# Kernel tuning notes

Hardware: AMD Instinct MI355X
Metric: run time of the kernel (lower is better)

The kernel has to match this reference:

```python
import jax, jax.numpy as jnp
import numpy as np

N_PAIR = 45  # n_agents=10 -> 10*9/2
TINY_THR = np.sqrt(np.finfo(np.float32).tiny).astype(np.float32) * N_PAIR


def setup_inputs() -> dict:
    key = jax.random.key(0)
    ks = jax.random.split(key, 8)
    bs, T, din, H = 4096, 64, 512, 64
    s = lambda fan: 1.0 / np.sqrt(fan)
    return {
        "main": jax.random.normal(ks[0], (1, bs, T, din), jnp.float32),
        "hidden_states": jnp.zeros((1, bs, 1, H), jnp.float32),
        "epsilons": jax.random.uniform(ks[1], (bs, 1), jnp.float32),
        "W_fc1": jax.random.normal(ks[2], (H, din), jnp.float32) * s(din),
        "b_fc1": jnp.zeros((H,), jnp.float32),
        "W_ih": jax.random.normal(ks[3], (3 * H, H), jnp.float32) * s(H),
        "W_hh": jax.random.normal(ks[4], (3 * H, H), jnp.float32) * s(H),
        "b_ih": jnp.zeros((3 * H,), jnp.float32),
        "b_hh": jnp.zeros((3 * H,), jnp.float32),
        "W_out": jax.random.normal(ks[5], (N_PAIR, H), jnp.float32) * s(H),
        "b_out": jnp.zeros((N_PAIR,), jnp.float32),
    }


def reference(main, hidden_states, epsilons, W_fc1, b_fc1, W_ih, W_hh, b_ih, b_hh, W_out, b_out):
    x = main[0]                       # [bs, T, din]
    h0 = hidden_states[0, :, 0, :]    # [bs, H]
    H = h0.shape[-1]

    # Encoder: fc1 + relu (time-independent, fully batched)
    enc = jax.nn.relu(jnp.einsum('bti,oi->bto', x, W_fc1) + b_fc1)  # [bs,T,H]
    # Precompute input-side GRU gates for all timesteps
    gi = jnp.einsum('bth,gh->btg', enc, W_ih) + b_ih                # [bs,T,3H]
    gi_t = jnp.transpose(gi, (1, 0, 2))                             # [T,bs,3H]

    def step(h, g_in):
        gh = h @ W_hh.T + b_hh
        i_r, i_z, i_n = jnp.split(g_in, 3, axis=-1)
        h_r, h_z, h_n = jnp.split(gh, 3, axis=-1)
        r = jax.nn.sigmoid(i_r + h_r)
        z = jax.nn.sigmoid(i_z + h_z)
        n = jnp.tanh(i_n + r * h_n)
        h_new = (1.0 - z) * n + z * h
        return h_new, h_new

    _, hs = jax.lax.scan(step, h0, gi_t)          # hs: [T,bs,H]
    hs = jnp.transpose(hs, (1, 0, 2))             # [bs,T,H]

    # Output head + custom exp-normalize with zero-sum guard
    logits = jnp.einsum('bth,oh->bto', hs, W_out) + b_out  # [bs,T,N_PAIR]
    p = jnp.exp(logits)
    p_sum = jnp.sum(p, axis=-1, keepdims=True)
    p_sum = jnp.where(p_sum <= TINY_THR, 1.0, p_sum)
    p = p / p_sum

    # Epsilon-greedy mixing (softmax exploration, not test_mode)
    eps = epsilons[:, None, :]                    # [bs,1,1]
    p = eps / N_PAIR + p * (1.0 - eps)

    x_out = p[None]                               # [1,bs,T,N_PAIR]
    h_out = hs[None]                              # [1,bs,T,H]
    return (x_out, h_out)
```

## Files before the change

### kernel.cpp

```cpp
#include <hip/hip_runtime.h>

typedef __attribute__((ext_vector_type(4))) float  f32x4;
typedef __attribute__((ext_vector_type(4))) __bf16 bf16x4;
typedef __attribute__((ext_vector_type(8))) __bf16 bf16x8;

#define MFMA16 __builtin_amdgcn_mfma_f32_16x16x32_bf16
#define TINY_THR 4.8789098e-18f
#define XOUT_N ((size_t)4096 * 64 * 45)

__device__ __forceinline__ void bar_lds() {
  asm volatile("s_waitcnt lgkmcnt(0)\n\ts_barrier" ::: "memory");
}
__device__ __forceinline__ void split_bf16(float v, __bf16& h, __bf16& l) {
  h = (__bf16)v; l = (__bf16)(v - (float)h);
}
__device__ __forceinline__ void gll16(const void* g, void* l) {
  __builtin_amdgcn_global_load_lds(
      (const __attribute__((address_space(1))) void*)g,
      (__attribute__((address_space(3))) void*)l, 16, 0, 0);
}

__device__ __forceinline__ int pk_off(int row, int col) {
  const int kk = col >> 5, rem = col & 31;
  const int half = rem >> 4, qq = (rem >> 2) & 3, j = rem & 3;
  return row * 128 + ((((kk << 2) | qq) ^ (row & 7)) << 4) + half * 8 + j * 2;
}
__device__ __forceinline__ bf16x8 frag_pk(const char* base, int row, int kk, int qq) {
  return *(const bf16x8*)(base + row * 128 + ((((kk << 2) | qq) ^ (row & 7)) << 4));
}

__global__ void k_prepW(const float* __restrict__ Wfc, __bf16* __restrict__ Wpk) {
  const int idx = blockIdx.x * 256 + threadIdx.x;
  const float v = Wfc[idx];
  __bf16 h, l; split_bf16(v, h, l);
  const int row = idx >> 9, k = idx & 511;
  const int c = k >> 6, kl = k & 63;
  const int kk = kl >> 5, rem = kl & 31;
  const int half = rem >> 4, q = (rem >> 2) & 3, j = rem & 3;
  const int blk = ((kk << 2) | q) ^ (row & 7);
  const int pos = c * 8192 + row * 64 + blk * 8 + half * 4 + j;
  Wpk[pos] = h;
  Wpk[pos + 4096] = l;
}

__global__ __launch_bounds__(256, 2) void k_encgemm(
    const float* __restrict__ x, const __bf16* __restrict__ Wpk,
    const float* __restrict__ bfc, float* __restrict__ enc) {
  __shared__ __attribute__((aligned(16))) char sm[65536];
  const int tid  = threadIdx.x;
  const int lane = tid & 63;
  const int wv   = tid >> 6;
  const int fr   = lane & 15;
  const int q    = lane >> 4;
  const int b    = blockIdx.x;

  auto stage = [&](int c, int buf) {
    char* xbase = sm + buf * 16384;
    char* wbase = sm + 32768 + buf * 16384;
    #pragma unroll
    for (int i = 0; i < 4; ++i) {
      const int B   = wv * 256 + i * 64 + lane;
      const int row = B >> 4, blk = B & 15;
      const int bp  = blk ^ (row & 15);
      const int colb = ((bp >> 3) << 5) | ((bp & 1) << 4) | (((bp >> 1) & 3) << 2);
      const float* src = x + ((size_t)b * 64 + row) * 512 + c * 64 + colb;
      gll16(src, xbase + wv * 4096 + i * 1024);
    }
    #pragma unroll
    for (int i = 0; i < 4; ++i) {
      const __bf16* srcw = Wpk + c * 8192 + wv * 2048 + i * 512 + lane * 8;
      gll16(srcw, wbase + wv * 4096 + i * 1024);
    }
  };

  f32x4 acc[4];
  #pragma unroll
  for (int nt = 0; nt < 4; ++nt) acc[nt] = (f32x4){0.f, 0.f, 0.f, 0.f};

  stage(0, 0);
  int buf = 0;
  for (int c = 0; c < 8; ++c) {
    if (c < 7) {
      stage(c + 1, buf ^ 1);
      asm volatile("s_waitcnt vmcnt(8)\n\ts_barrier" ::: "memory");
    } else {
      asm volatile("s_waitcnt vmcnt(0)\n\ts_barrier" ::: "memory");
    }
    const char* xbase = sm + buf * 16384;
    const char* wbase = sm + 32768 + buf * 16384;
    const int arow = wv * 16 + fr;
    bf16x8 Ah[2], Al[2];
    #pragma unroll
    for (int kk = 0; kk < 2; ++kk) {
      f32x4 u0 = *(const f32x4*)(xbase + arow * 256 + (((kk * 8 + q * 2 + 0) ^ (arow & 15)) << 4));
      f32x4 u1 = *(const f32x4*)(xbase + arow * 256 + (((kk * 8 + q * 2 + 1) ^ (arow & 15)) << 4));
      #pragma unroll
      for (int j = 0; j < 4; ++j) {
        __bf16 h, l;
        split_bf16(u0[j], h, l); Ah[kk][j] = h;     Al[kk][j] = l;
        split_bf16(u1[j], h, l); Ah[kk][4 + j] = h; Al[kk][4 + j] = l;
      }
    }
    #pragma unroll
    for (int nt = 0; nt < 4; ++nt) {
      const int brow = nt * 16 + fr;
      #pragma unroll
      for (int kk = 0; kk < 2; ++kk) {
        bf16x8 Bh = frag_pk(wbase, brow, kk, q);
        bf16x8 Bl = frag_pk(wbase + 8192, brow, kk, q);
        acc[nt] = MFMA16(Ah[kk], Bh, acc[nt], 0, 0, 0);
        acc[nt] = MFMA16(Ah[kk], Bl, acc[nt], 0, 0, 0);
        acc[nt] = MFMA16(Al[kk], Bh, acc[nt], 0, 0, 0);
      }
    }
    bar_lds();
    buf ^= 1;
  }
  #pragma unroll
  for (int nt = 0; nt < 4; ++nt) {
    const int o = nt * 16 + fr;
    const float bb = bfc[o];
    #pragma unroll
    for (int e = 0; e < 4; ++e) {
      const int t = wv * 16 + q * 4 + e;
      float v = acc[nt][e] + bb;
      enc[((size_t)b * 64 + t) * 64 + o] = fmaxf(v, 0.f);
    }
  }
}

__global__ __launch_bounds__(512, 1) void k_scan(
    const float* __restrict__ enc, const float* __restrict__ h0g,
    const float* __restrict__ eps, const float* __restrict__ Wih,
    const float* __restrict__ Whh, const float* __restrict__ bih,
    const float* __restrict__ bhh, const float* __restrict__ Wout,
    const float* __restrict__ bout, float* __restrict__ xout,
    float* __restrict__ hout) {
  __shared__ __attribute__((aligned(16))) char sm[55808];
  char* const wst0 = sm;
  char* const wst1 = sm + 24576;

  const int tid  = threadIdx.x;
  const int lane = tid & 63;
  const int wv   = tid >> 6;
  const int fr   = lane & 15;
  const int q    = lane >> 4;
  const int bbase = blockIdx.x * 16;
  const bool isB = (wv < 4);
  const int aw  = wv - 4;
  const int at  = tid & 255;
  const int sb  = at >> 4;
  const int sub = at & 15;
  const int so  = sub << 2;

  float hreg[4] = {0.f, 0.f, 0.f, 0.f};
  float biasNh = 0.f;
  int hcol = 0;
  float bR_ = 0.f, bZ_ = 0.f, bN_ = 0.f, boutv = 0.f, epsv = 0.f;
  if (isB) {
    hcol = wv * 16 + fr;
    biasNh = bhh[128 + hcol];
    #pragma unroll
    for (int e = 0; e < 4; ++e)
      hreg[e] = h0g[(size_t)(bbase + q * 4 + e) * 64 + hcol];
  } else {
    const int gc = aw * 16 + fr;
    bR_ = bih[gc] + bhh[gc];
    bZ_ = bih[64 + gc] + bhh[64 + gc];
    bN_ = bih[128 + gc];
    if (aw < 3 && gc < 45) boutv = bout[gc];
    epsv = eps[bbase + sb];
  }

  bf16x8 Fh[3][2], Fl[3][2];
  bf16x8 Fout[2][2];

  for (int idx = tid; idx < 192 * 64; idx += 512) {
    __bf16 h, l; split_bf16(Wih[idx], h, l);
    const int off = pk_off(idx >> 6, idx & 63);
    *(__bf16*)(wst0 + off) = h;
    *(__bf16*)(wst1 + off) = l;
  }
  bar_lds();
  if (!isB) {
    #pragma unroll
    for (int t3 = 0; t3 < 3; ++t3)
      #pragma unroll
      for (int kk = 0; kk < 2; ++kk) {
        const int row = (aw + 4 * t3) * 16 + fr;
        Fh[t3][kk] = frag_pk(wst0, row, kk, q);
        Fl[t3][kk] = frag_pk(wst1, row, kk, q);
      }
  }
  bar_lds();
  for (int idx = tid; idx < 192 * 64; idx += 512) {
    __bf16 h, l; split_bf16(Whh[idx], h, l);
    const int off = pk_off(idx >> 6, idx & 63);
    *(__bf16*)(wst0 + off) = h;
    *(__bf16*)(wst1 + off) = l;
  }
  bar_lds();
  if (isB) {
    #pragma unroll
    for (int t3 = 0; t3 < 3; ++t3)
      #pragma unroll
      for (int kk = 0; kk < 2; ++kk) {
        const int row = (wv + 4 * t3) * 16 + fr;
        Fh[t3][kk] = frag_pk(wst0, row, kk, q);
        Fl[t3][kk] = frag_pk(wst1, row, kk, q);
      }
  }
  bar_lds();
  for (int idx = tid; idx < 48 * 64; idx += 512) {
    float v = (idx < 45 * 64) ? Wout[idx] : 0.f;
    __bf16 h, l; split_bf16(v, h, l);
    const int off = pk_off(idx >> 6, idx & 63);
    *(__bf16*)(wst0 + off) = h;
    *(__bf16*)(wst1 + off) = l;
  }
  bar_lds();
  if (!isB && aw < 3) {
    #pragma unroll
    for (int kk = 0; kk < 2; ++kk) {
      const int row = aw * 16 + fr;
      Fout[kk][0] = frag_pk(wst0, row, kk, q);
      Fout[kk][1] = frag_pk(wst1, row, kk, q);
    }
  }
  bar_lds();

  auto gate_mfma = [&](const char* s0, f32x4& a0, f32x4& a1, f32x4& a2) {
    const char* s1 = s0 + 2048;
    bf16x8 Sh[2], Sl[2];
    #pragma unroll
    for (int kk = 0; kk < 2; ++kk) {
      Sh[kk] = frag_pk(s0, fr, kk, q);
      Sl[kk] = frag_pk(s1, fr, kk, q);
    }
    __builtin_amdgcn_s_setprio(1);
    #pragma unroll
    for (int kk = 0; kk < 2; ++kk) {
      a0 = MFMA16(Sh[kk], Fh[0][kk], a0, 0, 0, 0);
      a0 = MFMA16(Sh[kk], Fl[0][kk], a0, 0, 0, 0);
      a0 = MFMA16(Sl[kk], Fh[0][kk], a0, 0, 0, 0);
      a1 = MFMA16(Sh[kk], Fh[1][kk], a1, 0, 0, 0);
      a1 = MFMA16(Sh[kk], Fl[1][kk], a1, 0, 0, 0);
      a1 = MFMA16(Sl[kk], Fh[1][kk], a1, 0, 0, 0);
      a2 = MFMA16(Sh[kk], Fh[2][kk], a2, 0, 0, 0);
      a2 = MFMA16(Sh[kk], Fl[2][kk], a2, 0, 0, 0);
      a2 = MFMA16(Sl[kk], Fh[2][kk], a2, 0, 0, 0);
    }
    __builtin_amdgcn_s_setprio(0);
  };
  auto put_epd = [&](int dst, const f32x4& ev) {
    bf16x4 h4, l4;
    #pragma unroll
    for (int j = 0; j < 4; ++j) { __bf16 h, l; split_bf16(ev[j], h, l); h4[j] = h; l4[j] = l; }
    char* p0 = sm + 8192 + dst * 4096;
    const int off = pk_off(sb, so);
    *(bf16x4*)(p0 + off) = h4;
    *(bf16x4*)(p0 + 2048 + off) = l4;
  };
  auto put_gi = [&](int dst, const f32x4& a0, const f32x4& a1, const f32x4& a2) {
    float* gw = (float*)(sm + 16384 + dst * 16640);
    const int gc = aw * 16 + fr;
    #pragma unroll
    for (int e = 0; e < 4; ++e) {
      f32x4 o = (f32x4){a0[e] + bR_, a1[e] + bZ_, a2[e] + bN_, 0.f};
      *(f32x4*)(gw + (q * 4 + e) * 260 + gc * 4) = o;
    }
  };

  f32x4 evA = (f32x4){0.f,0.f,0.f,0.f}, evB = evA, e1v = evA;
  if (isB) {
    char* h0b = sm;
    char* h1b = sm + 2048;
    #pragma unroll
    for (int e = 0; e < 4; ++e) {
      __bf16 h, l; split_bf16(hreg[e], h, l);
      const int off = pk_off(q * 4 + e, hcol);
      *(__bf16*)(h0b + off) = h;
      *(__bf16*)(h1b + off) = l;
    }
  } else {
    const float* eb = enc + (size_t)(bbase + sb) * 64 * 64 + so;
    f32x4 e0v = *(const f32x4*)(eb);
    e1v = *(const f32x4*)(eb + 64);
    evA = *(const f32x4*)(eb + 2 * 64);
    evB = *(const f32x4*)(eb + 3 * 64);
    put_epd(1, e0v);
  }
  bar_lds();
  if (!isB) {
    f32x4 a0 = (f32x4){0.f,0.f,0.f,0.f}, a1 = a0, a2 = a0;
    gate_mfma(sm + 8192 + 1 * 4096, a0, a1, a2);
    put_gi(0, a0, a1, a2);
    put_epd(0, e1v);
  }
  bar_lds();

  auto body = [&](int t, int cur, f32x4& evC) {
    f32x4 a0 = (f32x4){0.f,0.f,0.f,0.f}, a1 = a0, a2 = a0;
    float giN[4];
    const char* s0;
    if (isB) {
      const float* gr = (const float*)(sm + 16384 + cur * 16640);
      #pragma unroll
      for (int e = 0; e < 4; ++e) {
        f32x4 gv = *(const f32x4*)(gr + (q * 4 + e) * 260 + hcol * 4);
        a0[e] = gv[0]; a1[e] = gv[1]; giN[e] = gv[2];
      }
      s0 = sm + cur * 4096;
    } else {
      s0 = sm + 8192 + cur * 4096;
    }
    const bool doMain = isB ? (t <= 63) : (t <= 62);
    if (doMain) gate_mfma(s0, a0, a1, a2);

    if (isB) {
      if (t <= 63) {
        char* n0 = sm + (cur ^ 1) * 4096;
        char* n1 = n0 + 2048;
        #pragma unroll
        for (int e = 0; e < 4; ++e) {
          const float rr = 1.f / (1.f + __expf(-a0[e]));
          const float zz = 1.f / (1.f + __expf(-a1[e]));
          const float npre = giN[e] + rr * (a2[e] + biasNh);
          const float nn = 2.f / (1.f + __expf(-2.f * npre)) - 1.f;
          const float hv = (1.f - zz) * nn + zz * hreg[e];
          hreg[e] = hv;
          hout[((size_t)(bbase + q * 4 + e) * 64 + t) * 64 + hcol] = hv;
          __bf16 h, l; split_bf16(hv, h, l);
          const int off = pk_off(q * 4 + e, hcol);
          *(__bf16*)(n0 + off) = h;
          *(__bf16*)(n1 + off) = l;
        }
      }
    } else {
      if (t <= 62) put_gi(cur ^ 1, a0, a1, a2);
      if (t >= 1 && t <= 64 && aw < 3) {
        const char* hp0c = sm + cur * 4096;
        const char* hp1c = hp0c + 2048;
        bf16x8 Hh[2], Hl[2];
        #pragma unroll
        for (int kk = 0; kk < 2; ++kk) {
          Hh[kk] = frag_pk(hp0c, fr, kk, q);
          Hl[kk] = frag_pk(hp1c, fr, kk, q);
        }
        f32x4 lacc = (f32x4){0.f, 0.f, 0.f, 0.f};
        #pragma unroll
        for (int kk = 0; kk < 2; ++kk) {
          lacc = MFMA16(Hh[kk], Fout[kk][0], lacc, 0, 0, 0);
          lacc = MFMA16(Hh[kk], Fout[kk][1], lacc, 0, 0, 0);
          lacc = MFMA16(Hl[kk], Fout[kk][0], lacc, 0, 0, 0);
        }
        float* lg = (float*)(sm + 49664 + (cur ^ 1) * 3072);
        #pragma unroll
        for (int e = 0; e < 4; ++e)
          lg[(q * 4 + e) * 48 + aw * 16 + fr] = lacc[e] + boutv;
      }
      if (t <= 61) put_epd(cur ^ 1, evC);
      if (t <= 59)
        evC = *(const f32x4*)(enc + ((size_t)(bbase + sb) * 64 + (t + 4)) * 64 + so);
      if (t >= 2) {
        const float* lg = (const float*)(sm + 49664 + cur * 3072);
        const float e0 = __expf(lg[sb * 48 + sub]);
        const float e1 = (sub + 16 < 45) ? __expf(lg[sb * 48 + sub + 16]) : 0.f;
        const float e2 = (sub + 32 < 45) ? __expf(lg[sb * 48 + sub + 32]) : 0.f;
        float s = e0 + e1 + e2;
        s += __shfl_xor(s, 1, 16);
        s += __shfl_xor(s, 2, 16);
        s += __shfl_xor(s, 4, 16);
        s += __shfl_xor(s, 8, 16);
        if (s <= TINY_THR) s = 1.f;
        const float sc  = (1.f - epsv) / s;
        const float bse = epsv * (1.f / 45.f);
        float* orow = xout + ((size_t)(bbase + sb) * 64 + (t - 2)) * 45;
        orow[sub] = bse + e0 * sc;
        if (sub + 16 < 45) orow[sub + 16] = bse + e1 * sc;
        if (sub + 32 < 45) orow[sub + 32] = bse + e2 * sc;
      }
    }
    bar_lds();
  };

  for (int t2 = 0; t2 < 66; t2 += 2) {
    body(t2, 0, evA);
    body(t2 + 1, 1, evB);
  }
}

extern "C" void kernel_launch(void* const* d_in, const int* in_sizes, int n_in,
                              void* d_out, int out_size, void* d_ws, size_t ws_size,
                              hipStream_t stream) {
  (void)in_sizes; (void)n_in; (void)out_size; (void)d_ws; (void)ws_size;
  const float* x    = (const float*)d_in[0];
  const float* h0   = (const float*)d_in[1];
  const float* eps  = (const float*)d_in[2];
  const float* Wfc  = (const float*)d_in[3];
  const float* bfc  = (const float*)d_in[4];
  const float* Wih  = (const float*)d_in[5];
  const float* Whh  = (const float*)d_in[6];
  const float* bih  = (const float*)d_in[7];
  const float* bhh  = (const float*)d_in[8];
  const float* Wout = (const float*)d_in[9];
  const float* bout = (const float*)d_in[10];

  float* xout = (float*)d_out;
  float* hout = xout + XOUT_N;
  float* enc = hout;
  __bf16* Wpk = (__bf16*)d_out;

  k_prepW<<<128, 256, 0, stream>>>(Wfc, Wpk);
  k_encgemm<<<4096, 256, 0, stream>>>(x, Wpk, bfc, enc);
  k_scan<<<256, 512, 0, stream>>>(enc, h0, eps, Wih, Whh, bih, bhh, Wout, bout,
                                  xout, hout);
}
```

Before: 241.1 us.

## Halve batch rows per scan block to launch twice as many blocks

The GRU scan kernel now gives each block 8 batch rows instead of 16 and launches 512 blocks, so more CUs take part in the serial 64-step recurrence. MFMA tiles stay 16 rows wide, with the unused rows zero-padded and masked out. The output-projection weights move from registers into a dedicated LDS region, and the launch bound is relaxed to allow more blocks per CU. The cost is half-wasted MFMA work, extra LDS reads each step and larger shared memory per block.

```diff
diff --git a/kernel.cpp b/kernel.cpp
--- a/kernel.cpp
+++ b/kernel.cpp
@@ -129,29 +129,33 @@
   }
 }
 
-__global__ __launch_bounds__(512, 1) void k_scan(
+__global__ __launch_bounds__(512, 4) void k_scan(
     const float* __restrict__ enc, const float* __restrict__ h0g,
     const float* __restrict__ eps, const float* __restrict__ Wih,
     const float* __restrict__ Whh, const float* __restrict__ bih,
     const float* __restrict__ bhh, const float* __restrict__ Wout,
     const float* __restrict__ bout, float* __restrict__ xout,
     float* __restrict__ hout) {
-  __shared__ __attribute__((aligned(16))) char sm[55808];
+  __shared__ __attribute__((aligned(16))) char sm[61440];
   char* const wst0 = sm;
   char* const wst1 = sm + 24576;
+  char* const wo0  = sm + 49152;
+  char* const wo1  = sm + 55296;
 
   const int tid  = threadIdx.x;
   const int lane = tid & 63;
   const int wv   = tid >> 6;
   const int fr   = lane & 15;
   const int q    = lane >> 4;
-  const int bbase = blockIdx.x * 16;
+  const int bbase = blockIdx.x * 8;
   const bool isB = (wv < 4);
   const int aw  = wv - 4;
   const int at  = tid & 255;
   const int sb  = at >> 4;
   const int sub = at & 15;
   const int so  = sub << 2;
+  const bool sbv = sb < 8;
+  const bool qv  = q < 2;
 
   float hreg[4] = {0.f, 0.f, 0.f, 0.f};
   float biasNh = 0.f;
@@ -160,20 +164,21 @@
   if (isB) {
     hcol = wv * 16 + fr;
     biasNh = bhh[128 + hcol];
-    #pragma unroll
-    for (int e = 0; e < 4; ++e)
-      hreg[e] = h0g[(size_t)(bbase + q * 4 + e) * 64 + hcol];
+    if (qv) {
+      #pragma unroll
+      for (int e = 0; e < 4; ++e)
+        hreg[e] = h0g[(size_t)(bbase + q * 4 + e) * 64 + hcol];
+    }
   } else {
     const int gc = aw * 16 + fr;
     bR_ = bih[gc] + bhh[gc];
     bZ_ = bih[64 + gc] + bhh[64 + gc];
     bN_ = bih[128 + gc];
     if (aw < 3 && gc < 45) boutv = bout[gc];
-    epsv = eps[bbase + sb];
+    if (sbv) epsv = eps[bbase + sb];
   }
 
   bf16x8 Fh[3][2], Fl[3][2];
-  bf16x8 Fout[2][2];
 
   for (int idx = tid; idx < 192 * 64; idx += 512) {
     __bf16 h, l; split_bf16(Wih[idx], h, l);
@@ -199,6 +204,13 @@
     *(__bf16*)(wst0 + off) = h;
     *(__bf16*)(wst1 + off) = l;
   }
+  for (int idx = tid; idx < 48 * 64; idx += 512) {
+    float v = (idx < 45 * 64) ? Wout[idx] : 0.f;
+    __bf16 h, l; split_bf16(v, h, l);
+    const int off = pk_off(idx >> 6, idx & 63);
+    *(__bf16*)(wo0 + off) = h;
+    *(__bf16*)(wo1 + off) = l;
+  }
   bar_lds();
   if (isB) {
     #pragma unroll
@@ -209,23 +221,6 @@
         Fh[t3][kk] = frag_pk(wst0, row, kk, q);
         Fl[t3][kk] = frag_pk(wst1, row, kk, q);
       }
-  }
-  bar_lds();
-  for (int idx = tid; idx < 48 * 64; idx += 512) {
-    float v = (idx < 45 * 64) ? Wout[idx] : 0.f;
-    __bf16 h, l; split_bf16(v, h, l);
-    const int off = pk_off(idx >> 6, idx & 63);
-    *(__bf16*)(wst0 + off) = h;
-    *(__bf16*)(wst1 + off) = l;
-  }
-  bar_lds();
-  if (!isB && aw < 3) {
-    #pragma unroll
-    for (int kk = 0; kk < 2; ++kk) {
-      const int row = aw * 16 + fr;
-      Fout[kk][0] = frag_pk(wst0, row, kk, q);
-      Fout[kk][1] = frag_pk(wst1, row, kk, q);
-    }
   }
   bar_lds();
 
@@ -262,7 +257,8 @@
     *(bf16x4*)(p0 + 2048 + off) = l4;
   };
   auto put_gi = [&](int dst, const f32x4& a0, const f32x4& a1, const f32x4& a2) {
-    float* gw = (float*)(sm + 16384 + dst * 16640);
+    if (!qv) return;
+    float* gw = (float*)(sm + 16384 + dst * 8320);
     const int gc = aw * 16 + fr;
     #pragma unroll
     for (int e = 0; e < 4; ++e) {
@@ -273,21 +269,26 @@
 
   f32x4 evA = (f32x4){0.f,0.f,0.f,0.f}, evB = evA, e1v = evA;
   if (isB) {
-    char* h0b = sm;
-    char* h1b = sm + 2048;
     #pragma unroll
     for (int e = 0; e < 4; ++e) {
       __bf16 h, l; split_bf16(hreg[e], h, l);
       const int off = pk_off(q * 4 + e, hcol);
-      *(__bf16*)(h0b + off) = h;
-      *(__bf16*)(h1b + off) = l;
+      *(__bf16*)(sm + off) = h;
+      *(__bf16*)(sm + 2048 + off) = l;
+      if (!qv) {
+        *(__bf16*)(sm + 4096 + off) = (__bf16)0.f;
+        *(__bf16*)(sm + 6144 + off) = (__bf16)0.f;
+      }
     }
   } else {
-    const float* eb = enc + (size_t)(bbase + sb) * 64 * 64 + so;
-    f32x4 e0v = *(const f32x4*)(eb);
-    e1v = *(const f32x4*)(eb + 64);
-    evA = *(const f32x4*)(eb + 2 * 64);
-    evB = *(const f32x4*)(eb + 3 * 64);
+    f32x4 e0v = (f32x4){0.f,0.f,0.f,0.f};
+    if (sbv) {
+      const float* eb = enc + (size_t)(bbase + sb) * 64 * 64 + so;
+      e0v = *(const f32x4*)(eb);
+      e1v = *(const f32x4*)(eb + 64);
+      evA = *(const f32x4*)(eb + 2 * 64);
+      evB = *(const f32x4*)(eb + 3 * 64);
+    }
     put_epd(1, e0v);
   }
   bar_lds();
@@ -301,14 +302,14 @@
 
   auto body = [&](int t, int cur, f32x4& evC) {
     f32x4 a0 = (f32x4){0.f,0.f,0.f,0.f}, a1 = a0, a2 = a0;
-    float giN[4];
+    f32x4 gv[4];
     const char* s0;
     if (isB) {
-      const float* gr = (const float*)(sm + 16384 + cur * 16640);
-      #pragma unroll
-      for (int e = 0; e < 4; ++e) {
-        f32x4 gv = *(const f32x4*)(gr + (q * 4 + e) * 260 + hcol * 4);
-        a0[e] = gv[0]; a1[e] = gv[1]; giN[e] = gv[2];
+      if (qv) {
+        const float* gr = (const float*)(sm + 16384 + cur * 8320);
+        #pragma unroll
+        for (int e = 0; e < 4; ++e)
+          gv[e] = *(const f32x4*)(gr + (q * 4 + e) * 260 + hcol * 4);
       }
       s0 = sm + cur * 4096;
     } else {
@@ -318,14 +319,14 @@
     if (doMain) gate_mfma(s0, a0, a1, a2);
 
     if (isB) {
-      if (t <= 63) {
+      if (t <= 63 && qv) {
         char* n0 = sm + (cur ^ 1) * 4096;
         char* n1 = n0 + 2048;
         #pragma unroll
         for (int e = 0; e < 4; ++e) {
-          const float rr = 1.f / (1.f + __expf(-a0[e]));
-          const float zz = 1.f / (1.f + __expf(-a1[e]));
-          const float npre = giN[e] + rr * (a2[e] + biasNh);
+          const float rr = 1.f / (1.f + __expf(-(a0[e] + gv[e][0])));
+          const float zz = 1.f / (1.f + __expf(-(a1[e] + gv[e][1])));
+          const float npre = gv[e][2] + rr * (a2[e] + biasNh);
           const float nn = 2.f / (1.f + __expf(-2.f * npre)) - 1.f;
           const float hv = (1.f - zz) * nn + zz * hreg[e];
           hreg[e] = hv;
@@ -341,29 +342,28 @@
       if (t >= 1 && t <= 64 && aw < 3) {
         const char* hp0c = sm + cur * 4096;
         const char* hp1c = hp0c + 2048;
-        bf16x8 Hh[2], Hl[2];
-        #pragma unroll
-        for (int kk = 0; kk < 2; ++kk) {
-          Hh[kk] = frag_pk(hp0c, fr, kk, q);
-          Hl[kk] = frag_pk(hp1c, fr, kk, q);
-        }
+        const int wrow = aw * 16 + fr;
         f32x4 lacc = (f32x4){0.f, 0.f, 0.f, 0.f};
         #pragma unroll
         for (int kk = 0; kk < 2; ++kk) {
-          lacc = MFMA16(Hh[kk], Fout[kk][0], lacc, 0, 0, 0);
-          lacc = MFMA16(Hh[kk], Fout[kk][1], lacc, 0, 0, 0);
-          lacc = MFMA16(Hl[kk], Fout[kk][0], lacc, 0, 0, 0);
+          bf16x8 Hh = frag_pk(hp0c, fr, kk, q);
+          bf16x8 Hl = frag_pk(hp1c, fr, kk, q);
+          bf16x8 Foh = frag_pk(wo0, wrow, kk, q);
+          bf16x8 Fol = frag_pk(wo1, wrow, kk, q);
+          lacc = MFMA16(Hh, Foh, lacc, 0, 0, 0);
+          lacc = MFMA16(Hh, Fol, lacc, 0, 0, 0);
+          lacc = MFMA16(Hl, Foh, lacc, 0, 0, 0);
         }
-        float* lg = (float*)(sm + 49664 + (cur ^ 1) * 3072);
+        float* lg = (float*)(sm + 33024 + (cur ^ 1) * 3072);
         #pragma unroll
         for (int e = 0; e < 4; ++e)
           lg[(q * 4 + e) * 48 + aw * 16 + fr] = lacc[e] + boutv;
       }
       if (t <= 61) put_epd(cur ^ 1, evC);
-      if (t <= 59)
+      if (t <= 59 && sbv)
         evC = *(const f32x4*)(enc + ((size_t)(bbase + sb) * 64 + (t + 4)) * 64 + so);
-      if (t >= 2) {
-        const float* lg = (const float*)(sm + 49664 + cur * 3072);
+      if (t >= 2 && sbv) {
+        const float* lg = (const float*)(sm + 33024 + cur * 3072);
         const float e0 = __expf(lg[sb * 48 + sub]);
         const float e1 = (sub + 16 < 45) ? __expf(lg[sb * 48 + sub + 16]) : 0.f;
         const float e2 = (sub + 32 < 45) ? __expf(lg[sb * 48 + sub + 32]) : 0.f;
@@ -413,6 +413,6 @@
 
   k_prepW<<<128, 256, 0, stream>>>(Wfc, Wpk);
   k_encgemm<<<4096, 256, 0, stream>>>(x, Wpk, bfc, enc);
-  k_scan<<<256, 512, 0, stream>>>(enc, h0, eps, Wih, Whh, bih, bhh, Wout, bout,
+  k_scan<<<512, 512, 0, stream>>>(enc, h0, eps, Wih, Whh, bih, bhh, Wout, bout,
                                   xout, hout);
 }
```

Result: slower. 393.9 us (+63.4%).
